# Kernel optimization log

Measured on AMD Instinct MI355X. Metric: run time of the kernel, lower is better.

Reference implementation:

```python
import jax, jax.numpy as jnp
import numpy as np

NPERSEG = 128  # configs.nperseg
NREF = 32      # configs.nref
EPS = 1e-12


def _frames(x, nperseg, step):
    nseg = (x.shape[-1] - (nperseg - step)) // step
    idx = jnp.arange(nseg)[:, None] * step + jnp.arange(nperseg)[None, :]
    return x[..., idx]


def _welch_fft(x, nperseg):
    # Welch-style segmented, constant-detrended, Hann-windowed rfft
    step = nperseg - nperseg // 2  # noverlap = nperseg // 2
    f = _frames(x, nperseg, step)
    f = f - f.mean(axis=-1, keepdims=True)  # detrend='constant'
    win = 0.5 - 0.5 * jnp.cos(2.0 * jnp.pi * jnp.arange(nperseg) / nperseg)  # periodic Hann
    return jnp.fft.rfft(f * win, axis=-1)  # [..., S, F] complex


def setup_inputs() -> dict:
    key = jax.random.key(0)
    k1, k2 = jax.random.split(key)
    B, C_T, L, N = 8, 16, 2048, 2048
    target_series = jax.random.normal(k1, (B, C_T, L), dtype=jnp.float32)
    TS_database = jax.random.normal(k2, (B, N, L), dtype=jnp.float32)
    return {"target_series": target_series, "TS_database": TS_database}


def reference(target_series, TS_database):
    B, C_T, L = target_series.shape
    N = TS_database.shape[1]
    # nref <= N, so we take the coherence-scoring branch
    X = _welch_fft(target_series, NPERSEG)  # [B, C, S, F]
    Y = _welch_fft(TS_database, NPERSEG)    # [B, N, S, F]
    S = X.shape[-2]
    Pxx = jnp.mean(jnp.abs(X) ** 2, axis=-2)                      # [B, C, F]
    Pyy = jnp.mean(jnp.abs(Y) ** 2, axis=-2)                      # [B, N, F]
    Pxy = jnp.einsum('bcsf,bnsf->bcnf', X, jnp.conj(Y)) / S      # [B, C, N, F]
    coh = (jnp.abs(Pxy) ** 2) / (Pxx[:, :, None, :] * Pyy[:, None, :, :] + EPS)
    scores = coh.mean(axis=-1)                                    # [B, C, N]
    _, topk_idx = jax.lax.top_k(scores, NREF)                     # [B, C, K]
    # gather: db [B,1,N,L], idx [B,C,K,1] -> [B,C,K,L] (broadcasting take_along_axis)
    gathered = jnp.take_along_axis(TS_database[:, None, :, :], topk_idx[..., None], axis=2)
    return gathered.reshape(B, C_T * NREF, L)
```

## Files before the change

### kernel.cpp

```cpp
#include <hip/hip_runtime.h>

#define BQ 8
#define CQ 16
#define LQ 2048
#define NQ 2048
#define NPS 128
#define STEPQ 64
#define SQ 31
#define FQ 65
#define KQ 32
#define EPSQ 1e-12f

#define XQ_OFF     0ull
#define XTAIL_OFF  2031616ull
#define PXX_OFF    2063360ull
#define SCORES_OFF 2096640ull
#define TOPK_OFF   3145216ull

#define YLD 66
#define OFF_Y     0
#define OFF_PYY   4092
#define OFF_RED   4157
#define SMEM_FLOATS 4413

#define C16R(j) ((j)==0?1.0f:(j)==1?0.92387953251128675613f:(j)==2?0.70710678118654752440f:\
    (j)==3?0.38268343236508977173f:(j)==4?0.0f:(j)==5?-0.38268343236508977173f:\
    (j)==6?-0.70710678118654752440f:(j)==7?-0.92387953251128675613f:(j)==8?-1.0f:\
    (j)==9?-0.92387953251128675613f:(j)==10?-0.70710678118654752440f:(j)==11?-0.38268343236508977173f:\
    (j)==12?0.0f:(j)==13?0.38268343236508977173f:(j)==14?0.70710678118654752440f:0.92387953251128675613f)
#define C16I(j) (-((j)==0?0.0f:(j)==1?0.38268343236508977173f:(j)==2?0.70710678118654752440f:\
    (j)==3?0.92387953251128675613f:(j)==4?1.0f:(j)==5?0.92387953251128675613f:\
    (j)==6?0.70710678118654752440f:(j)==7?0.38268343236508977173f:(j)==8?0.0f:\
    (j)==9?-0.38268343236508977173f:(j)==10?-0.70710678118654752440f:(j)==11?-0.92387953251128675613f:\
    (j)==12?-1.0f:(j)==13?-0.92387953251128675613f:(j)==14?-0.70710678118654752440f:-0.38268343236508977173f))

__device__ __constant__ const float WA_R[8] = {1.f, 1.f, 1.f, 1.f,
    1.f, 0.70710678118654752440f, 0.f, -0.70710678118654752440f};
__device__ __constant__ const float WA_I[8] = {0.f, 0.f, 0.f, 0.f,
    0.f, -0.70710678118654752440f, -1.f, -0.70710678118654752440f};
__device__ __constant__ const int BR3_[8] = {0, 4, 2, 6, 1, 5, 3, 7};

#define TWOPI_128 0.049087385212340519350978802863742f

__device__ __forceinline__ float dppx1(float v) {
    return __int_as_float(__builtin_amdgcn_update_dpp(0, __float_as_int(v), 0xB1, 0xF, 0xF, true));
}
__device__ __forceinline__ float dppx2(float v) {
    return __int_as_float(__builtin_amdgcn_update_dpp(0, __float_as_int(v), 0x4E, 0xF, 0xF, true));
}

__device__ __forceinline__ float2 pk_cma1(float2 x, float2 y, float2 acc) {
    float2 d;
    asm("v_pk_fma_f32 %0, %1, %2, %3 op_sel:[0,0,0] op_sel_hi:[1,0,1]"
        : "=v"(d) : "v"(x), "v"(y), "v"(acc));
    return d;
}
__device__ __forceinline__ float2 pk_cma2(float2 x, float2 y, float2 acc) {
    float2 d;
    asm("v_pk_fma_f32 %0, %1, %2, %3 op_sel:[1,1,0] op_sel_hi:[0,1,1] neg_hi:[1,0,0]"
        : "=v"(d) : "v"(x), "v"(y), "v"(acc));
    return d;
}
__device__ __forceinline__ float2 pk_dft_lo(float2 xp, float2 w, float2 g) {
    float2 d;
    asm("v_pk_fma_f32 %0, %1, %2, %3 op_sel:[0,0,0] op_sel_hi:[0,1,1]"
        : "=v"(d) : "v"(xp), "s"(w), "v"(g));
    return d;
}
__device__ __forceinline__ float2 pk_dft_hi(float2 xp, float2 w, float2 g) {
    float2 d;
    asm("v_pk_fma_f32 %0, %1, %2, %3 op_sel:[1,0,0] op_sel_hi:[1,1,1]"
        : "=v"(d) : "v"(xp), "s"(w), "v"(g));
    return d;
}

__device__ __forceinline__ void welch_spectra(const float* __restrict__ grow,
                                              float* smem) {
    const int tid = threadIdx.x;
    float2* s_y = (float2*)(smem + OFF_Y);

    const bool act = tid < SQ * 8;
    const int s = tid >> 3, t1 = tid & 7;

    float x[16];
    float sum = 0.f;
    if (act) {
        const float* rp = grow + s * STEPQ + t1;
#pragma unroll
        for (int t2 = 0; t2 < 16; ++t2) x[t2] = rp[8 * t2];
#pragma unroll
        for (int t2 = 0; t2 < 16; ++t2) sum += x[t2];
    }
    sum += dppx1(sum);
    sum += dppx2(sum);
    sum += __shfl_xor(sum, 4, 64);
    const float mean = sum * (1.0f / 128.0f);

    float2 G[9];
    if (act) {
        float2 xp[8];
#pragma unroll
        for (int t2 = 0; t2 < 16; ++t2) {
            const float a = (float)(t1 + 8 * t2) * TWOPI_128;
            x[t2] = (x[t2] - mean) * (0.5f - 0.5f * __cosf(a));
        }
#pragma unroll
        for (int j = 0; j < 8; ++j) xp[j] = make_float2(x[2 * j], x[2 * j + 1]);
#pragma unroll
        for (int m = 0; m < 9; ++m) {
            float2 g = make_float2(0.f, 0.f);
#pragma unroll
            for (int j = 0; j < 8; ++j) {
                {
                    const int i0 = (m * (2 * j)) & 15;
                    g = pk_dft_lo(xp[j], make_float2(C16R(i0), C16I(i0)), g);
                }
                {
                    const int i1 = (m * (2 * j + 1)) & 15;
                    g = pk_dft_hi(xp[j], make_float2(C16R(i1), C16I(i1)), g);
                }
            }
            G[m] = g;
        }
    }

    const float s1 = (t1 & 4) ? -1.f : 1.f;
    const float s2 = (t1 & 2) ? -1.f : 1.f;
    const float s3 = (t1 & 1) ? -1.f : 1.f;
    const float war = WA_R[t1], wai = WA_I[t1];
    const bool q3 = (t1 & 3) == 3;
    const int kbase = 16 * BR3_[t1];

    float cr, ci;
    __sincosf((float)t1 * TWOPI_128, &ci, &cr);
    ci = -ci;
    float wr = 1.f, wi = 0.f;

    if (act) {
#pragma unroll
        for (int mp = 0; mp < 16; ++mp) {
            const int mm = (mp <= 8) ? mp : 16 - mp;
            const float sg = (mp <= 8) ? 1.f : -1.f;
            const float gr = G[mm].x, gi = sg * G[mm].y;
            float hr = wr * gr - wi * gi;
            float hi = wr * gi + wi * gr;
            float orr = __shfl_xor(hr, 4, 64), oi = __shfl_xor(hi, 4, 64);
            float vr = fmaf(s1, hr, orr), vi = fmaf(s1, hi, oi);
            hr = vr * war - vi * wai;
            hi = vr * wai + vi * war;
            orr = dppx2(hr); oi = dppx2(hi);
            vr = fmaf(s2, hr, orr); vi = fmaf(s2, hi, oi);
            hr = q3 ? vi : vr;
            hi = q3 ? -vr : vi;
            orr = dppx1(hr); oi = dppx1(hi);
            vr = fmaf(s3, hr, orr); vi = fmaf(s3, hi, oi);
            const int k = mp + kbase;
            if (k <= 64) s_y[s * YLD + k] = make_float2(vr, vi);
            const float nwr = wr * cr - wi * ci;
            wi = wr * ci + wi * cr;
            wr = nwr;
        }
    }
    __syncthreads();
}

__global__ __launch_bounds__(256) void k_xspec(const float* __restrict__ tgt,
                                               float2* __restrict__ xquad,
                                               float2* __restrict__ xtail,
                                               float* __restrict__ pxx) {
    __shared__ float smem[SMEM_FLOATS];
    const int blk = blockIdx.x;
    const int b = blk >> 4, c = blk & 15;
    welch_spectra(tgt + (size_t)blk * LQ, smem);
    const float2* s_y = (const float2*)(smem + OFF_Y);
    const int tid = threadIdx.x;
    for (int i = tid; i < SQ * FQ; i += 256) {
        const int s2 = i / 65, k = i - 65 * s2;
        const float2 v = s_y[s2 * YLD + k];
        if (k < 64) {
            const int q = k >> 2, j = k & 3;
            xquad[((((size_t)b * 16 + q) * SQ + s2) * CQ + c) * 4 + j] = v;
        } else {
            xtail[((size_t)b * SQ + s2) * CQ + c] = v;
        }
    }
    if (tid < FQ) {
        float a = 0.f;
        for (int s = 0; s < SQ; ++s) {
            const float2 y = s_y[s * YLD + tid];
            a += y.x * y.x + y.y * y.y;
        }
        pxx[(size_t)blk * FQ + tid] = a * (1.0f / (float)SQ);
    }
}

__global__ __launch_bounds__(256) void k_score(const float* __restrict__ db,
                                               const float2* __restrict__ xquad,
                                               const float2* __restrict__ xtail,
                                               const float* __restrict__ pxx,
                                               float* __restrict__ scores) {
    __shared__ float smem[SMEM_FLOATS];
    const int blk = blockIdx.x;
    const int b = blk >> 11, n = blk & 2047;
    welch_spectra(db + (size_t)blk * LQ, smem);
    float* s_pyy = smem + OFF_PYY;
    float* s_red = smem + OFF_RED;
    const int tid = threadIdx.x;

    if (tid < FQ) {
        float a = 0.f;
        for (int s = 0; s < SQ; ++s) {
            const float2 y = ((const float2*)(smem + OFF_Y))[s * YLD + tid];
            a += y.x * y.x + y.y * y.y;
        }
        s_pyy[tid] = a * (1.0f / (float)SQ);
    }
    __syncthreads();

    const int c = tid & 15, g = tid >> 4;
    const int f0 = 4 * g;
    const float4* xp = (const float4*)xquad + (((size_t)(b * 16 + g) * SQ) * CQ + c) * 2;
    const float*  px = pxx + ((size_t)b * CQ + c) * FQ;

    float2 a0 = make_float2(0.f, 0.f), a1 = a0, a2 = a0, a3 = a0;

    for (int s = 0; s < SQ; ++s) {
        const float4* yp = (const float4*)(smem + OFF_Y + (size_t)(s * YLD + f0) * 2);
        const float4 ya = yp[0];
        const float4 yb = yp[1];
        const float4 xa = xp[0];
        const float4 xb4 = xp[1];
        xp += 32;
        const float2 x0 = make_float2(xa.x, xa.y), x1 = make_float2(xa.z, xa.w);
        const float2 x2 = make_float2(xb4.x, xb4.y), x3 = make_float2(xb4.z, xb4.w);
        const float2 y0 = make_float2(ya.x, ya.y), y1 = make_float2(ya.z, ya.w);
        const float2 y2 = make_float2(yb.x, yb.y), y3 = make_float2(yb.z, yb.w);
        a0 = pk_cma1(x0, y0, a0);  a0 = pk_cma2(x0, y0, a0);
        a1 = pk_cma1(x1, y1, a1);  a1 = pk_cma2(x1, y1, a1);
        a2 = pk_cma1(x2, y2, a2);  a2 = pk_cma2(x2, y2, a2);
        a3 = pk_cma1(x3, y3, a3);  a3 = pk_cma2(x3, y3, a3);
    }
    const float invS2 = 1.0f / ((float)SQ * (float)SQ);
    float acc = 0.f;
    acc += ((a0.x * a0.x + a0.y * a0.y) * invS2) / (px[f0 + 0] * s_pyy[f0 + 0] + EPSQ);
    acc += ((a1.x * a1.x + a1.y * a1.y) * invS2) / (px[f0 + 1] * s_pyy[f0 + 1] + EPSQ);
    acc += ((a2.x * a2.x + a2.y * a2.y) * invS2) / (px[f0 + 2] * s_pyy[f0 + 2] + EPSQ);
    acc += ((a3.x * a3.x + a3.y * a3.y) * invS2) / (px[f0 + 3] * s_pyy[f0 + 3] + EPSQ);

    if (g == 0) {
        float2 a4 = make_float2(0.f, 0.f);
        const float2* xt = xtail + (size_t)b * SQ * CQ + c;
        for (int s = 0; s < SQ; ++s) {
            const float2 y4 = ((const float2*)(smem + OFF_Y))[s * YLD + 64];
            const float2 x4 = xt[s * CQ];
            a4 = pk_cma1(x4, y4, a4);  a4 = pk_cma2(x4, y4, a4);
        }
        acc += ((a4.x * a4.x + a4.y * a4.y) * invS2) / (px[64] * s_pyy[64] + EPSQ);
    }

    s_red[tid] = acc;
    __syncthreads();
    if (tid < 16) {
        float a = 0.f;
#pragma unroll
        for (int gg = 0; gg < 16; ++gg) a += s_red[gg * 16 + tid];
        scores[((size_t)b * CQ + tid) * NQ + n] = a * (1.0f / (float)FQ);
    }
}

__global__ __launch_bounds__(256) void k_topk(const float* __restrict__ scores,
                                              int* __restrict__ topk) {
    __shared__ float sv[NQ];
    __shared__ float rv[4];
    __shared__ int   ri[4];
    const int blk = blockIdx.x, tid = threadIdx.x;
    const float* row = scores + (size_t)blk * NQ;
    for (int i = tid; i < NQ; i += 256) sv[i] = row[i];
    __syncthreads();
    for (int k = 0; k < KQ; ++k) {
        float best = -3.402823466e38f;
        int bi = 0x7fffffff;
        for (int j = tid; j < NQ; j += 256) {
            const float v = sv[j];
            if (v > best) { best = v; bi = j; }
        }
#pragma unroll
        for (int off = 1; off < 64; off <<= 1) {
            const float ov = __shfl_xor(best, off, 64);
            const int   oi = __shfl_xor(bi, off, 64);
            if (ov > best || (ov == best && oi < bi)) { best = ov; bi = oi; }
        }
        if ((tid & 63) == 0) { rv[tid >> 6] = best; ri[tid >> 6] = bi; }
        __syncthreads();
        if (tid == 0) {
            float bv = rv[0]; int bj = ri[0];
#pragma unroll
            for (int w = 1; w < 4; ++w) {
                if (rv[w] > bv || (rv[w] == bv && ri[w] < bj)) { bv = rv[w]; bj = ri[w]; }
            }
            topk[blk * KQ + k] = bj;
            sv[bj] = -3.402823466e38f;
        }
        __syncthreads();
    }
}

__global__ __launch_bounds__(256) void k_gather(const float* __restrict__ db,
                                                const int* __restrict__ topk,
                                                float* __restrict__ out) {
    const int row = blockIdx.x;
    const int b = row >> 9;
    const int idx = topk[row];
    const float4* src = (const float4*)(db + ((size_t)(b * NQ + idx)) * LQ);
    float4* dst = (float4*)(out + (size_t)row * LQ);
    const int tid = threadIdx.x;
    dst[tid] = src[tid];
    dst[tid + 256] = src[tid + 256];
}

extern "C" void kernel_launch(void* const* d_in, const int* in_sizes, int n_in,
                              void* d_out, int out_size, void* d_ws, size_t ws_size,
                              hipStream_t stream) {
    const float* tgt = (const float*)d_in[0];
    const float* db  = (const float*)d_in[1];
    float* out = (float*)d_out;
    char* ws = (char*)d_ws;

    float2* xquad  = (float2*)(ws + XQ_OFF);
    float2* xtail  = (float2*)(ws + XTAIL_OFF);
    float*  pxx    = (float*)(ws + PXX_OFF);
    float*  scores = (float*)(ws + SCORES_OFF);
    int*    topk   = (int*)(ws + TOPK_OFF);

    hipLaunchKernelGGL(k_xspec,  dim3(BQ * CQ),      dim3(256), 0, stream, tgt, xquad, xtail, pxx);
    hipLaunchKernelGGL(k_score,  dim3(BQ * NQ),      dim3(256), 0, stream, db, xquad, xtail, pxx, scores);
    hipLaunchKernelGGL(k_topk,   dim3(BQ * CQ),      dim3(256), 0, stream, scores, topk);
    hipLaunchKernelGGL(k_gather, dim3(BQ * CQ * KQ), dim3(256), 0, stream, db, topk, out);
}
```

Measured before the change: 469.3 us.

## Pad spectrum LDS rows, tabulate Hann window, swizzle shuffle, register top-k

Several independent micro-optimizations. The shared spectrum buffer gets one float2 of padding every 16 bins to reduce LDS bank conflicts in the FFT writeback and in later reads. The Hann window is computed once into a workspace table by k_xspec and loaded by k_score instead of evaluating cosines per element. The xor-4 shuffle becomes a ds_swizzle, and top-k keeps its candidates in registers instead of LDS. Unaligned float2 LDS reads in the score loop replace the earlier float4 reads, which could cost bandwidth.

```diff
diff --git a/kernel.cpp b/kernel.cpp
--- a/kernel.cpp
+++ b/kernel.cpp
@@ -16,12 +16,13 @@
 #define PXX_OFF    2063360ull
 #define SCORES_OFF 2096640ull
 #define TOPK_OFF   3145216ull
-
-#define YLD 66
+#define WTAB_OFF   3177984ull
+
+#define YLD 69
 #define OFF_Y     0
-#define OFF_PYY   4092
-#define OFF_RED   4157
-#define SMEM_FLOATS 4413
+#define OFF_PYY   4278
+#define OFF_RED   4343
+#define SMEM_FLOATS 4599
 
 #define C16R(j) ((j)==0?1.0f:(j)==1?0.92387953251128675613f:(j)==2?0.70710678118654752440f:\
     (j)==3?0.38268343236508977173f:(j)==4?0.0f:(j)==5?-0.38268343236508977173f:\
@@ -48,6 +49,9 @@
 __device__ __forceinline__ float dppx2(float v) {
     return __int_as_float(__builtin_amdgcn_update_dpp(0, __float_as_int(v), 0x4E, 0xF, 0xF, true));
 }
+__device__ __forceinline__ float swzx4(float v) {
+    return __int_as_float(__builtin_amdgcn_ds_swizzle(__float_as_int(v), 0x101F));
+}
 
 __device__ __forceinline__ float2 pk_cma1(float2 x, float2 y, float2 acc) {
     float2 d;
@@ -74,7 +78,9 @@
     return d;
 }
 
+template<bool TAB>
 __device__ __forceinline__ void welch_spectra(const float* __restrict__ grow,
+                                              const float* __restrict__ wtab,
                                               float* smem) {
     const int tid = threadIdx.x;
     float2* s_y = (float2*)(smem + OFF_Y);
@@ -93,7 +99,7 @@
     }
     sum += dppx1(sum);
     sum += dppx2(sum);
-    sum += __shfl_xor(sum, 4, 64);
+    sum += swzx4(sum);
     const float mean = sum * (1.0f / 128.0f);
 
     float2 G[9];
@@ -101,8 +107,14 @@
         float2 xp[8];
 #pragma unroll
         for (int t2 = 0; t2 < 16; ++t2) {
-            const float a = (float)(t1 + 8 * t2) * TWOPI_128;
-            x[t2] = (x[t2] - mean) * (0.5f - 0.5f * __cosf(a));
+            float wv;
+            if (TAB) {
+                wv = wtab[t1 + 8 * t2];
+            } else {
+                const float a = (float)(t1 + 8 * t2) * TWOPI_128;
+                wv = 0.5f - 0.5f * __cosf(a);
+            }
+            x[t2] = (x[t2] - mean) * wv;
         }
 #pragma unroll
         for (int j = 0; j < 8; ++j) xp[j] = make_float2(x[2 * j], x[2 * j + 1]);
@@ -129,7 +141,7 @@
     const float s3 = (t1 & 1) ? -1.f : 1.f;
     const float war = WA_R[t1], wai = WA_I[t1];
     const bool q3 = (t1 & 3) == 3;
-    const int kbase = 16 * BR3_[t1];
+    const int pbase = 17 * BR3_[t1];
 
     float cr, ci;
     __sincosf((float)t1 * TWOPI_128, &ci, &cr);
@@ -137,6 +149,7 @@
     float wr = 1.f, wi = 0.f;
 
     if (act) {
+        float2* yrow = s_y + s * YLD + pbase;
 #pragma unroll
         for (int mp = 0; mp < 16; ++mp) {
             const int mm = (mp <= 8) ? mp : 16 - mp;
@@ -144,7 +157,7 @@
             const float gr = G[mm].x, gi = sg * G[mm].y;
             float hr = wr * gr - wi * gi;
             float hi = wr * gi + wi * gr;
-            float orr = __shfl_xor(hr, 4, 64), oi = __shfl_xor(hi, 4, 64);
+            float orr = swzx4(hr), oi = swzx4(hi);
             float vr = fmaf(s1, hr, orr), vi = fmaf(s1, hi, oi);
             hr = vr * war - vi * wai;
             hi = vr * wai + vi * war;
@@ -154,8 +167,7 @@
             hi = q3 ? -vr : vi;
             orr = dppx1(hr); oi = dppx1(hi);
             vr = fmaf(s3, hr, orr); vi = fmaf(s3, hi, oi);
-            const int k = mp + kbase;
-            if (k <= 64) s_y[s * YLD + k] = make_float2(vr, vi);
+            if (pbase + mp <= 68) yrow[mp] = make_float2(vr, vi);
             const float nwr = wr * cr - wi * ci;
             wi = wr * ci + wi * cr;
             wr = nwr;
@@ -167,16 +179,19 @@
 __global__ __launch_bounds__(256) void k_xspec(const float* __restrict__ tgt,
                                                float2* __restrict__ xquad,
                                                float2* __restrict__ xtail,
-                                               float* __restrict__ pxx) {
+                                               float* __restrict__ pxx,
+                                               float* __restrict__ wtab) {
     __shared__ float smem[SMEM_FLOATS];
     const int blk = blockIdx.x;
     const int b = blk >> 4, c = blk & 15;
-    welch_spectra(tgt + (size_t)blk * LQ, smem);
+    const int tid = threadIdx.x;
+    if (blk == 0 && tid < NPS)
+        wtab[tid] = 0.5f - 0.5f * __cosf((float)tid * TWOPI_128);
+    welch_spectra<false>(tgt + (size_t)blk * LQ, nullptr, smem);
     const float2* s_y = (const float2*)(smem + OFF_Y);
-    const int tid = threadIdx.x;
     for (int i = tid; i < SQ * FQ; i += 256) {
         const int s2 = i / 65, k = i - 65 * s2;
-        const float2 v = s_y[s2 * YLD + k];
+        const float2 v = s_y[s2 * YLD + k + (k >> 4)];
         if (k < 64) {
             const int q = k >> 2, j = k & 3;
             xquad[((((size_t)b * 16 + q) * SQ + s2) * CQ + c) * 4 + j] = v;
@@ -185,9 +200,10 @@
         }
     }
     if (tid < FQ) {
+        const int pc = tid + (tid >> 4);
         float a = 0.f;
         for (int s = 0; s < SQ; ++s) {
-            const float2 y = s_y[s * YLD + tid];
+            const float2 y = s_y[s * YLD + pc];
             a += y.x * y.x + y.y * y.y;
         }
         pxx[(size_t)blk * FQ + tid] = a * (1.0f / (float)SQ);
@@ -198,19 +214,22 @@
                                                const float2* __restrict__ xquad,
                                                const float2* __restrict__ xtail,
                                                const float* __restrict__ pxx,
+                                               const float* __restrict__ wtab,
                                                float* __restrict__ scores) {
     __shared__ float smem[SMEM_FLOATS];
     const int blk = blockIdx.x;
     const int b = blk >> 11, n = blk & 2047;
-    welch_spectra(db + (size_t)blk * LQ, smem);
+    welch_spectra<true>(db + (size_t)blk * LQ, wtab, smem);
     float* s_pyy = smem + OFF_PYY;
     float* s_red = smem + OFF_RED;
     const int tid = threadIdx.x;
+    const float2* yall = (const float2*)(smem + OFF_Y);
 
     if (tid < FQ) {
+        const int pc = tid + (tid >> 4);
         float a = 0.f;
         for (int s = 0; s < SQ; ++s) {
-            const float2 y = ((const float2*)(smem + OFF_Y))[s * YLD + tid];
+            const float2 y = yall[s * YLD + pc];
             a += y.x * y.x + y.y * y.y;
         }
         s_pyy[tid] = a * (1.0f / (float)SQ);
@@ -219,22 +238,20 @@
 
     const int c = tid & 15, g = tid >> 4;
     const int f0 = 4 * g;
+    const int p0 = f0 + (f0 >> 4);
     const float4* xp = (const float4*)xquad + (((size_t)(b * 16 + g) * SQ) * CQ + c) * 2;
     const float*  px = pxx + ((size_t)b * CQ + c) * FQ;
 
     float2 a0 = make_float2(0.f, 0.f), a1 = a0, a2 = a0, a3 = a0;
 
     for (int s = 0; s < SQ; ++s) {
-        const float4* yp = (const float4*)(smem + OFF_Y + (size_t)(s * YLD + f0) * 2);
-        const float4 ya = yp[0];
-        const float4 yb = yp[1];
+        const float2* yb = yall + s * YLD + p0;
+        const float2 y0 = yb[0], y1 = yb[1], y2 = yb[2], y3 = yb[3];
         const float4 xa = xp[0];
         const float4 xb4 = xp[1];
         xp += 32;
         const float2 x0 = make_float2(xa.x, xa.y), x1 = make_float2(xa.z, xa.w);
         const float2 x2 = make_float2(xb4.x, xb4.y), x3 = make_float2(xb4.z, xb4.w);
-        const float2 y0 = make_float2(ya.x, ya.y), y1 = make_float2(ya.z, ya.w);
-        const float2 y2 = make_float2(yb.x, yb.y), y3 = make_float2(yb.z, yb.w);
         a0 = pk_cma1(x0, y0, a0);  a0 = pk_cma2(x0, y0, a0);
         a1 = pk_cma1(x1, y1, a1);  a1 = pk_cma2(x1, y1, a1);
         a2 = pk_cma1(x2, y2, a2);  a2 = pk_cma2(x2, y2, a2);
@@ -251,7 +268,7 @@
         float2 a4 = make_float2(0.f, 0.f);
         const float2* xt = xtail + (size_t)b * SQ * CQ + c;
         for (int s = 0; s < SQ; ++s) {
-            const float2 y4 = ((const float2*)(smem + OFF_Y))[s * YLD + 64];
+            const float2 y4 = yall[s * YLD + 68];
             const float2 x4 = xt[s * CQ];
             a4 = pk_cma1(x4, y4, a4);  a4 = pk_cma2(x4, y4, a4);
         }
@@ -270,19 +287,20 @@
 
 __global__ __launch_bounds__(256) void k_topk(const float* __restrict__ scores,
                                               int* __restrict__ topk) {
-    __shared__ float sv[NQ];
     __shared__ float rv[4];
     __shared__ int   ri[4];
+    __shared__ int   sbj;
     const int blk = blockIdx.x, tid = threadIdx.x;
     const float* row = scores + (size_t)blk * NQ;
-    for (int i = tid; i < NQ; i += 256) sv[i] = row[i];
-    __syncthreads();
+    float v[8];
+#pragma unroll
+    for (int j = 0; j < 8; ++j) v[j] = row[tid + 256 * j];
     for (int k = 0; k < KQ; ++k) {
         float best = -3.402823466e38f;
         int bi = 0x7fffffff;
-        for (int j = tid; j < NQ; j += 256) {
-            const float v = sv[j];
-            if (v > best) { best = v; bi = j; }
+#pragma unroll
+        for (int j = 0; j < 8; ++j) {
+            if (v[j] > best) { best = v[j]; bi = tid + 256 * j; }
         }
 #pragma unroll
         for (int off = 1; off < 64; off <<= 1) {
@@ -295,13 +313,17 @@
         if (tid == 0) {
             float bv = rv[0]; int bj = ri[0];
 #pragma unroll
-            for (int w = 1; w < 4; ++w) {
-                if (rv[w] > bv || (rv[w] == bv && ri[w] < bj)) { bv = rv[w]; bj = ri[w]; }
+            for (int w2 = 1; w2 < 4; ++w2) {
+                if (rv[w2] > bv || (rv[w2] == bv && ri[w2] < bj)) { bv = rv[w2]; bj = ri[w2]; }
             }
             topk[blk * KQ + k] = bj;
-            sv[bj] = -3.402823466e38f;
+            sbj = bj;
         }
         __syncthreads();
+        const int bj = sbj;
+#pragma unroll
+        for (int j = 0; j < 8; ++j)
+            if (bj == tid + 256 * j) v[j] = -3.402823466e38f;
     }
 }
 
@@ -331,9 +353,10 @@
     float*  pxx    = (float*)(ws + PXX_OFF);
     float*  scores = (float*)(ws + SCORES_OFF);
     int*    topk   = (int*)(ws + TOPK_OFF);
-
-    hipLaunchKernelGGL(k_xspec,  dim3(BQ * CQ),      dim3(256), 0, stream, tgt, xquad, xtail, pxx);
-    hipLaunchKernelGGL(k_score,  dim3(BQ * NQ),      dim3(256), 0, stream, db, xquad, xtail, pxx, scores);
+    float*  wtab   = (float*)(ws + WTAB_OFF);
+
+    hipLaunchKernelGGL(k_xspec,  dim3(BQ * CQ),      dim3(256), 0, stream, tgt, xquad, xtail, pxx, wtab);
+    hipLaunchKernelGGL(k_score,  dim3(BQ * NQ),      dim3(256), 0, stream, db, xquad, xtail, pxx, wtab, scores);
     hipLaunchKernelGGL(k_topk,   dim3(BQ * CQ),      dim3(256), 0, stream, scores, topk);
     hipLaunchKernelGGL(k_gather, dim3(BQ * CQ * KQ), dim3(256), 0, stream, db, topk, out);
 }
```

Result: faster. 457.0 us (-2.6%).
